# Kernel optimization log

Measured on AMD Instinct MI355X. Metric: run time of the kernel, lower is better.

Reference implementation:

```python
import jax, jax.numpy as jnp
import numpy as np

B, S, D_EMBED, D_HIDDEN = 4, 256, 300, 300
C = 5.0  # frozen tanh-scaling constant


def setup_inputs() -> dict:
    key = jax.random.key(0)
    ks = jax.random.split(key, 8)
    w = 0.05  # ~xavier scale for 300x300
    return {
        "inputs": jax.random.normal(ks[0], (B, S, D_EMBED), jnp.float32),
        "rep_mask": jax.random.randint(ks[1], (B, S), 0, 2, jnp.int32),
        "W_fc": jax.random.normal(ks[2], (D_HIDDEN, D_EMBED), jnp.float32) * w,
        "b_fc": jnp.zeros((D_HIDDEN,), jnp.float32),
        "W1": jax.random.normal(ks[3], (D_HIDDEN, D_HIDDEN), jnp.float32) * w,
        "W2": jax.random.normal(ks[4], (D_HIDDEN, D_HIDDEN), jnp.float32) * w,
        "b1": jnp.zeros((D_HIDDEN,), jnp.float32),
        "W_f1": jax.random.normal(ks[5], (D_HIDDEN, D_HIDDEN), jnp.float32) * w,
        "W_f2": jax.random.normal(ks[6], (D_HIDDEN, D_HIDDEN), jnp.float32) * w,
        "b_f": jnp.zeros((D_HIDDEN,), jnp.float32),
    }


def _disa_fwd(inputs, rep_mask_f, W_fc, b_fc, W1, W2, b1, W_f1, W_f2, b_f):
    n_seq = inputs.shape[1]
    # forward direction mask: attend to strictly later positions (triu, diag=1)
    direct = jnp.triu(jnp.ones((n_seq, n_seq), inputs.dtype), k=1)
    # mask[b,i,j] = rep_mask[b,j] * direct[i,j], shape [B,S,S,1]
    mask = (rep_mask_f[:, None, :] * direct[None]) [..., None]

    rep_map = jax.nn.elu(jnp.einsum('bse,he->bsh', inputs, W_fc) + b_fc)  # [B,S,D]
    dep = jnp.einsum('bsh,gh->bsg', rep_map, W1)   # dependent (token j)
    head = jnp.einsum('bsh,gh->bsg', rep_map, W2)  # head (token i)

    # logits[b,i,j,d]
    logits = C * jnp.tanh((dep[:, None, :, :] + head[:, :, None, :] + b1) / C)

    # hand-rolled masked softmax over dim=2 (j), faithful to original
    masked = logits * mask
    mx = jnp.max(masked, axis=2, keepdims=True)
    exps = jnp.exp(masked - mx) * mask
    sums = jnp.sum(exps, axis=2, keepdims=True)
    sums = sums + (sums == 0).astype(logits.dtype)
    attn = (exps / (sums + 1e-20)) * mask

    attn_result = jnp.sum(attn * rep_map[:, None, :, :], axis=2)  # [B,S,D]

    gate = jax.nn.sigmoid(
        jnp.einsum('bsh,gh->bsg', rep_map, W_f1)
        + jnp.einsum('bsh,gh->bsg', attn_result, W_f2)
        + b_f
    )
    out = gate * rep_map + (1.0 - gate) * attn_result
    return out * rep_mask_f[..., None]


def reference(inputs, rep_mask, W_fc, b_fc, W1, W2, b1, W_f1, W_f2, b_f):
    rep_mask_f = rep_mask.astype(inputs.dtype)
    return _disa_fwd(inputs, rep_mask_f, W_fc, b_fc, W1, W2, b1, W_f1, W_f2, b_f)
```

## Files before the change

### kernel.cpp

```cpp
#include <hip/hip_runtime.h>
#include <hip/hip_bf16.h>

#define Dx 300
#define Mx 1024

#define OFF_REP    0
#define OFF_DEP    307200
#define OFF_HEAD   614400
#define OFF_ATTN   921600
#define U_BASE     1228800
#define REPB       0
#define ATB        327680
#define WPACK      655360
#define WP1        655360
#define WP2        757760
#define WPF1       860160
#define WPF2       962560

typedef __attribute__((ext_vector_type(8))) short short8;
typedef __attribute__((ext_vector_type(4))) float f32x4;

union S8 { unsigned int u[4]; unsigned short s[8]; short8 v; };

__device__ __forceinline__ float bf2f(unsigned short u) {
    union { unsigned int i; float f; } v; v.i = ((unsigned int)u) << 16; return v.f;
}
__device__ __forceinline__ unsigned short f2bf(float x) {
    union { float f; unsigned int i; } u; u.f = x;
    return (unsigned short)((u.i + 0x8000u) >> 16);
}
__device__ __forceinline__ int detect_bf16(const void* w) {
    const unsigned short* u = (const unsigned short*)w;
    int ok = 1;
    #pragma unroll
    for (int t = 0; t < 64; ++t) { float v = bf2f(u[t]); ok &= (fabsf(v) < 1.0f) ? 1 : 0; }
    return ok;
}
__device__ __forceinline__ float ldf(const void* p, int idx, int isbf) {
    return isbf ? bf2f(((const unsigned short*)p)[idx]) : ((const float*)p)[idx];
}

__device__ __forceinline__ void load8f(const float* rowp, int kb, int kmax,
                                       int valid, float* x) {
    if (valid && kb + 8 <= kmax) {
        float4 a = *(const float4*)(rowp + kb);
        float4 b = *(const float4*)(rowp + kb + 4);
        x[0]=a.x; x[1]=a.y; x[2]=a.z; x[3]=a.w;
        x[4]=b.x; x[5]=b.y; x[6]=b.z; x[7]=b.w;
    } else {
        #pragma unroll
        for (int j = 0; j < 8; ++j) {
            int k = kb + j;
            x[j] = (valid && k < kmax) ? rowp[k] : 0.f;
        }
    }
}
__device__ __forceinline__ short8 pack8(const float* x) {
    S8 H;
    #pragma unroll
    for (int p = 0; p < 4; ++p) {
        union { float f; unsigned int i; } a, b;
        a.f = x[2*p]; b.f = x[2*p+1];
        H.u[p] = ((a.i + 0x8000u) >> 16) | ((b.i + 0x8000u) & 0xFFFF0000u);
    }
    return H.v;
}
__device__ __forceinline__ short8 load8bf(const unsigned short* rowp, int kb,
                                          int kmax, int valid) {
    S8 R;
    if (valid && kb + 8 <= kmax) {
        ushort4 a = *(const ushort4*)(rowp + kb);
        ushort4 b = *(const ushort4*)(rowp + kb + 4);
        R.s[0]=a.x; R.s[1]=a.y; R.s[2]=a.z; R.s[3]=a.w;
        R.s[4]=b.x; R.s[5]=b.y; R.s[6]=b.z; R.s[7]=b.w;
    } else {
        #pragma unroll
        for (int j = 0; j < 8; ++j) {
            int k = kb + j;
            R.s[j] = (valid && k < kmax) ? rowp[k] : (unsigned short)0;
        }
    }
    return R.v;
}
__device__ __forceinline__ short8 loadB(const void* W, int row, int kb, int isbf,
                                        int valid) {
    if (isbf) return load8bf((const unsigned short*)W + row * 300, kb, 300, valid);
    float t[8];
    load8f((const float*)W + row * 300, kb, 300, valid, t);
    return pack8(t);
}

__global__ __launch_bounds__(256) void k_mm1(
        const void* __restrict__ Xv, const void* __restrict__ Wfc,
        const void* __restrict__ bfc, const void* __restrict__ W1,
        const void* __restrict__ W2,  const void* __restrict__ Wf1,
        const void* __restrict__ Wf2, float* __restrict__ ws) {
    __shared__ int s_isbf;
    if (threadIdx.x == 0) s_isbf = detect_bf16(Wfc);
    __syncthreads();
    const int isbf = s_isbf;
    const int tid = threadIdx.x;
    unsigned short* U = (unsigned short*)(ws + U_BASE);

    if (blockIdx.x >= 320) {
        const unsigned int idx = (blockIdx.x - 320) * 256 + tid;
        const unsigned int mi = idx / 102400;
        const unsigned int rem = idx - mi * 102400;
        const int row = rem / 320, k = rem - (rem / 320) * 320;
        const void* src = (mi == 0) ? W1 : (mi == 1) ? W2 : (mi == 2) ? Wf1 : Wf2;
        float v = (row < 300 && k < 300) ? ldf(src, row * 300 + k, isbf) : 0.f;
        U[WPACK + idx] = f2bf(v);
        return;
    }

    const int w = tid >> 6, l = tid & 63;
    const int mt = blockIdx.x / 5, nt = blockIdx.x % 5;
    const int m0 = mt * 16, lm = l & 15, koff = (l >> 4) * 8;
    const int nrow = nt * 64 + w * 16 + lm;
    const int bval = nrow < 300;
    const int ncl = bval ? nrow : 0;
    f32x4 acc = {0.f, 0.f, 0.f, 0.f};
    if (isbf) {
        const unsigned short* Xp = (const unsigned short*)Xv + (m0 + lm) * 300;
        #pragma unroll
        for (int ks = 0; ks < 10; ++ks) {
            short8 a = load8bf(Xp, ks*32 + koff, 300, 1);
            short8 b = loadB(Wfc, ncl, ks*32 + koff, 1, bval);
            acc = __builtin_amdgcn_mfma_f32_16x16x32_bf16(a, b, acc, 0, 0, 0);
        }
    } else {
        const float* Xp = (const float*)Xv + (m0 + lm) * 300;
        #pragma unroll
        for (int ks = 0; ks < 10; ++ks) {
            float t[8]; load8f(Xp, ks*32 + koff, 300, 1, t);
            short8 a = pack8(t);
            short8 b = loadB(Wfc, ncl, ks*32 + koff, 0, bval);
            acc = __builtin_amdgcn_mfma_f32_16x16x32_bf16(a, b, acc, 0, 0, 0);
        }
    }
    if (bval) {
        float bb = ldf(bfc, nrow, isbf);
        #pragma unroll
        for (int r = 0; r < 4; ++r) {
            int mg = m0 + (l >> 4) * 4 + r;
            float v = acc[r] + bb;
            v = v > 0.f ? v : (__expf(v) - 1.f);
            ws[OFF_REP + mg * 300 + nrow] = v;
            U[REPB + mg * 320 + nrow] = f2bf(v);
        }
    } else {
        #pragma unroll
        for (int r = 0; r < 4; ++r) {
            int mg = m0 + (l >> 4) * 4 + r;
            U[REPB + mg * 320 + nrow] = 0;
        }
    }
}

__global__ __launch_bounds__(256) void k_mm2(
        const void* __restrict__ b1, const void* __restrict__ Wdet,
        float* __restrict__ ws) {
    __shared__ int s_isbf;
    if (threadIdx.x == 0) s_isbf = detect_bf16(Wdet);
    __syncthreads();
    const int isbf = s_isbf;
    const int tid = threadIdx.x, w = tid >> 6, l = tid & 63;
    const int mt = blockIdx.x / 10, nt = blockIdx.x % 10;
    const int m0 = mt * 16, lm = l & 15, koff = (l >> 4) * 8;
    const int ng = nt * 64 + w * 16 + lm;
    const int wsel = ng < 320;
    const int wrow = wsel ? ng : ng - 320;
    const unsigned short* U = (const unsigned short*)(ws + U_BASE);
    const unsigned short* ap = U + REPB + (m0 + lm) * 320 + koff;
    const unsigned short* bp = U + (wsel ? WP1 : WP2) + wrow * 320 + koff;
    f32x4 acc = {0.f, 0.f, 0.f, 0.f};
    #pragma unroll
    for (int ks = 0; ks < 10; ++ks) {
        short8 a = *(const short8*)(ap + ks * 32);
        short8 b = *(const short8*)(bp + ks * 32);
        acc = __builtin_amdgcn_mfma_f32_16x16x32_bf16(a, b, acc, 0, 0, 0);
    }
    if (ng < 300) {
        float bb = ldf(b1, ng, isbf);
        #pragma unroll
        for (int r = 0; r < 4; ++r) {
            int mg = m0 + (l >> 4) * 4 + r;
            ws[OFF_DEP + mg * 300 + ng] = __expf(0.4f * (acc[r] + bb));
        }
    } else if (ng >= 320 && ng < 620) {
        #pragma unroll
        for (int r = 0; r < 4; ++r) {
            int mg = m0 + (l >> 4) * 4 + r;
            ws[OFF_HEAD + mg * 300 + (ng - 320)] = acc[r];
        }
    }
}

__global__ __launch_bounds__(320) void k_attn(
        float* __restrict__ ws, const int* __restrict__ mask) {
    const float* exd  = ws + OFF_DEP;
    const float* head = ws + OFF_HEAD;
    const float* rep  = ws + OFF_REP;
    unsigned short* U = (unsigned short*)(ws + U_BASE);
    __shared__ unsigned short vlist[256];
    __shared__ int s_cnt, s_st0, s_st1;
    const int blk = blockIdx.x;
    const int b = blk >> 7;
    const int tile = blk & 127;
    const int uu = tile >> 1;
    const int i0 = (tile & 1) ? (254 - 2 * uu) : (2 * uu);
    const int tid = threadIdx.x;

    if (tid < 64) {
        int basec = 0, st0 = 0, st1 = 0;
        #pragma unroll
        for (int c = 0; c < 4; ++c) {
            const int j = c * 64 + tid;
            const int mv = mask[b * 256 + j] != 0;
            unsigned long long bal = __ballot(mv);
            int pos = basec + __popcll(bal & ((1ull << tid) - 1ull));
            if (mv) vlist[pos] = (unsigned short)j;
            if (tid == 0) {
                int lim0 = i0 - c * 64;
                if (lim0 >= 0)
                    st0 += __popcll(bal & (lim0 >= 63 ? ~0ull : ((2ull << lim0) - 1ull)));
                int lim1 = i0 + 1 - c * 64;
                if (lim1 >= 0)
                    st1 += __popcll(bal & (lim1 >= 63 ? ~0ull : ((2ull << lim1) - 1ull)));
            }
            basec += __popcll(bal);
        }
        if (tid == 0) { s_cnt = basec; s_st0 = st0; s_st1 = st1; }
    }
    __syncthreads();
    const int d = tid;
    const int base = b * 256;
    if (d >= 300) {
        U[ATB + (base + i0) * 320 + d] = 0;
        U[ATB + (base + i0 + 1) * 320 + d] = 0;
        return;
    }
    const int cnt = s_cnt, st0 = s_st0, st1 = s_st1;

    const float hv0 = head[(base + i0) * Dx + d];
    const float hv1 = head[(base + i0 + 1) * Dx + d];
    const float pw0 = __expf(0.4f * hv0);
    const float pw1 = __expf(0.4f * hv1);

    const float* ep = exd + base * Dx + d;
    const float* rp = rep + base * Dx + d;
    float s0 = 0.f, r0 = 0.f, s1 = 0.f, r1 = 0.f;
    if (st1 > st0) {
        const int j = vlist[st0];
        float ex = ep[j * Dx];
        float rv = rp[j * Dx];
        float u0 = fmaf(ex, pw0, 1.0f);
        float e0 = __expf(-10.0f * __builtin_amdgcn_rcpf(u0));
        s0 += e0; r0 = fmaf(e0, rv, r0);
    }
    #pragma unroll 4
    for (int t = st1; t < cnt; ++t) {
        const int j = vlist[t];
        float ex = ep[j * Dx];
        float rv = rp[j * Dx];
        float u0 = fmaf(ex, pw0, 1.0f);
        float u1 = fmaf(ex, pw1, 1.0f);
        float e0 = __expf(-10.0f * __builtin_amdgcn_rcpf(u0));
        float e1 = __expf(-10.0f * __builtin_amdgcn_rcpf(u1));
        s0 += e0; r0 = fmaf(e0, rv, r0);
        s1 += e1; r1 = fmaf(e1, rv, r1);
    }
    const float den0 = s0 + (s0 == 0.f ? 1.f : 0.f) + 1e-20f;
    const float den1 = s1 + (s1 == 0.f ? 1.f : 0.f) + 1e-20f;
    const float a0 = r0 / den0, a1 = r1 / den1;
    ws[OFF_ATTN + (base + i0) * Dx + d]     = a0;
    ws[OFF_ATTN + (base + i0 + 1) * Dx + d] = a1;
    U[ATB + (base + i0) * 320 + d]     = f2bf(a0);
    U[ATB + (base + i0 + 1) * 320 + d] = f2bf(a1);
}

__global__ __launch_bounds__(256) void k_mm3(
        const void* __restrict__ bfv, const void* __restrict__ Wdet,
        const int* __restrict__ mask, float* __restrict__ ws,
        void* __restrict__ outv) {
    __shared__ int s_isbf;
    if (threadIdx.x == 0) s_isbf = detect_bf16(Wdet);
    __syncthreads();
    const int isbf = s_isbf;
    const int tid = threadIdx.x, w = tid >> 6, l = tid & 63;
    const int mt = blockIdx.x / 5, nt = blockIdx.x % 5;
    const int m0 = mt * 16, lm = l & 15, koff = (l >> 4) * 8;
    const int nrow = nt * 64 + w * 16 + lm;
    const unsigned short* U = (const unsigned short*)(ws + U_BASE);
    const unsigned short* a1p = U + REPB + (m0 + lm) * 320 + koff;
    const unsigned short* a2p = U + ATB  + (m0 + lm) * 320 + koff;
    const unsigned short* b1p = U + WPF1 + nrow * 320 + koff;
    const unsigned short* b2p = U + WPF2 + nrow * 320 + koff;
    f32x4 acc = {0.f, 0.f, 0.f, 0.f};
    #pragma unroll
    for (int ks = 0; ks < 10; ++ks) {
        short8 a = *(const short8*)(a1p + ks * 32);
        short8 b = *(const short8*)(b1p + ks * 32);
        acc = __builtin_amdgcn_mfma_f32_16x16x32_bf16(a, b, acc, 0, 0, 0);
    }
    #pragma unroll
    for (int ks = 0; ks < 10; ++ks) {
        short8 a = *(const short8*)(a2p + ks * 32);
        short8 b = *(const short8*)(b2p + ks * 32);
        acc = __builtin_amdgcn_mfma_f32_16x16x32_bf16(a, b, acc, 0, 0, 0);
    }
    if (nrow < 300) {
        float bb = ldf(bfv, nrow, isbf);
        #pragma unroll
        for (int r = 0; r < 4; ++r) {
            int mg = m0 + (l >> 4) * 4 + r;
            float gp = acc[r] + bb;
            float gate = 1.0f / (1.0f + __expf(-gp));
            float rv = ws[OFF_REP  + mg * 300 + nrow];
            float av = ws[OFF_ATTN + mg * 300 + nrow];
            float res = (gate * rv + (1.0f - gate) * av) * (float)mask[mg];
            if (isbf) ((__hip_bfloat16*)outv)[mg * 300 + nrow] = __float2bfloat16(res);
            else      ((float*)outv)[mg * 300 + nrow] = res;
        }
    }
}

extern "C" void kernel_launch(void* const* d_in, const int* in_sizes, int n_in,
                              void* d_out, int out_size, void* d_ws, size_t ws_size,
                              hipStream_t stream) {
    const void* X   = d_in[0];
    const int*  msk = (const int*)d_in[1];
    const void* Wfc = d_in[2];
    const void* bfc = d_in[3];
    const void* W1  = d_in[4];
    const void* W2  = d_in[5];
    const void* b1  = d_in[6];
    const void* Wf1 = d_in[7];
    const void* Wf2 = d_in[8];
    const void* bfv = d_in[9];
    float* ws = (float*)d_ws;

    hipLaunchKernelGGL(k_mm1,  dim3(1920), dim3(256), 0, stream,
                       X, Wfc, bfc, W1, W2, Wf1, Wf2, ws);
    hipLaunchKernelGGL(k_mm2,  dim3(640), dim3(256), 0, stream, b1, Wfc, ws);
    hipLaunchKernelGGL(k_attn, dim3(512), dim3(320), 0, stream, ws, msk);
    hipLaunchKernelGGL(k_mm3,  dim3(320), dim3(256), 0, stream,
                       bfv, Wfc, msk, ws, d_out);
}
```

Before: 125.0 us.

## Fuse four kernels into one persistent kernel with software grid barriers

Result: slower. 476.5 us (+281.2%).

```diff
diff --git a/kernel.cpp b/kernel.cpp
--- a/kernel.cpp
+++ b/kernel.cpp
@@ -2,7 +2,6 @@
 #include <hip/hip_bf16.h>
 
 #define Dx 300
-#define Mx 1024
 
 #define OFF_REP    0
 #define OFF_DEP    307200
@@ -16,6 +15,7 @@
 #define WP2        757760
 #define WPF1       860160
 #define WPF2       962560
+#define SYNC_FOFF  2000000
 
 typedef __attribute__((ext_vector_type(8))) short short8;
 typedef __attribute__((ext_vector_type(4))) float f32x4;
@@ -90,237 +90,274 @@
     return pack8(t);
 }
 
-__global__ __launch_bounds__(256) void k_mm1(
-        const void* __restrict__ Xv, const void* __restrict__ Wfc,
-        const void* __restrict__ bfc, const void* __restrict__ W1,
-        const void* __restrict__ W2,  const void* __restrict__ Wf1,
-        const void* __restrict__ Wf2, float* __restrict__ ws) {
+__device__ __forceinline__ void gbar(float* ws, int idx, int nblk) {
+    __syncthreads();
+    if (threadIdx.x == 0) {
+        int* s = (int*)(ws + SYNC_FOFF) + idx * 32;
+        int a = __hip_atomic_fetch_add(s, 1, __ATOMIC_ACQ_REL,
+                                       __HIP_MEMORY_SCOPE_AGENT);
+        if (a == nblk - 1) {
+            __hip_atomic_store(s + 16, 1, __ATOMIC_RELEASE,
+                               __HIP_MEMORY_SCOPE_AGENT);
+        } else {
+            int t = 0;
+            while (__hip_atomic_load(s + 16, __ATOMIC_ACQUIRE,
+                                     __HIP_MEMORY_SCOPE_AGENT) == 0) {
+                __builtin_amdgcn_s_sleep(2);
+                if (++t > 400000) break;
+            }
+        }
+    }
+    __syncthreads();
+}
+
+__global__ __launch_bounds__(320, 4) void k_fused(
+        const void* __restrict__ Xv, const int* __restrict__ mask,
+        const void* __restrict__ Wfc, const void* __restrict__ bfc,
+        const void* __restrict__ W1,  const void* __restrict__ W2,
+        const void* __restrict__ b1v, const void* __restrict__ Wf1,
+        const void* __restrict__ Wf2, const void* __restrict__ bfv,
+        float* __restrict__ ws, void* __restrict__ outv) {
     __shared__ int s_isbf;
-    if (threadIdx.x == 0) s_isbf = detect_bf16(Wfc);
+    __shared__ unsigned short vlist[256];
+    __shared__ int s_cnt, s_st0, s_st1;
+
+    const int tid = threadIdx.x;
+    const int blk = blockIdx.x;
+    if (tid == 0) s_isbf = detect_bf16(Wfc);
     __syncthreads();
     const int isbf = s_isbf;
-    const int tid = threadIdx.x;
     unsigned short* U = (unsigned short*)(ws + U_BASE);
 
-    if (blockIdx.x >= 320) {
-        const unsigned int idx = (blockIdx.x - 320) * 256 + tid;
-        const unsigned int mi = idx / 102400;
-        const unsigned int rem = idx - mi * 102400;
-        const int row = rem / 320, k = rem - (rem / 320) * 320;
-        const void* src = (mi == 0) ? W1 : (mi == 1) ? W2 : (mi == 2) ? Wf1 : Wf2;
-        float v = (row < 300 && k < 300) ? ldf(src, row * 300 + k, isbf) : 0.f;
-        U[WPACK + idx] = f2bf(v);
-        return;
-    }
-
-    const int w = tid >> 6, l = tid & 63;
-    const int mt = blockIdx.x / 5, nt = blockIdx.x % 5;
-    const int m0 = mt * 16, lm = l & 15, koff = (l >> 4) * 8;
-    const int nrow = nt * 64 + w * 16 + lm;
-    const int bval = nrow < 300;
-    const int ncl = bval ? nrow : 0;
-    f32x4 acc = {0.f, 0.f, 0.f, 0.f};
-    if (isbf) {
-        const unsigned short* Xp = (const unsigned short*)Xv + (m0 + lm) * 300;
+    if (blk < 320) {
+        if (tid < 256) {
+            const int w = tid >> 6, l = tid & 63;
+            const int mt = blk / 5, nt = blk % 5;
+            const int m0 = mt * 16, lm = l & 15, koff = (l >> 4) * 8;
+            const int nrow = nt * 64 + w * 16 + lm;
+            const int bval = nrow < 300;
+            const int ncl = bval ? nrow : 0;
+            f32x4 acc = {0.f, 0.f, 0.f, 0.f};
+            if (isbf) {
+                const unsigned short* Xp = (const unsigned short*)Xv + (m0 + lm) * 300;
+                #pragma unroll
+                for (int ks = 0; ks < 10; ++ks) {
+                    short8 a = load8bf(Xp, ks*32 + koff, 300, 1);
+                    short8 b = loadB(Wfc, ncl, ks*32 + koff, 1, bval);
+                    acc = __builtin_amdgcn_mfma_f32_16x16x32_bf16(a, b, acc, 0, 0, 0);
+                }
+            } else {
+                const float* Xp = (const float*)Xv + (m0 + lm) * 300;
+                #pragma unroll
+                for (int ks = 0; ks < 10; ++ks) {
+                    float t[8]; load8f(Xp, ks*32 + koff, 300, 1, t);
+                    short8 a = pack8(t);
+                    short8 b = loadB(Wfc, ncl, ks*32 + koff, 0, bval);
+                    acc = __builtin_amdgcn_mfma_f32_16x16x32_bf16(a, b, acc, 0, 0, 0);
+                }
+            }
+            if (bval) {
+                float bb = ldf(bfc, nrow, isbf);
+                #pragma unroll
+                for (int r = 0; r < 4; ++r) {
+                    int mg = m0 + (l >> 4) * 4 + r;
+                    float v = acc[r] + bb;
+                    v = v > 0.f ? v : (__expf(v) - 1.f);
+                    ws[OFF_REP + mg * 300 + nrow] = v;
+                    U[REPB + mg * 320 + nrow] = f2bf(v);
+                }
+            } else {
+                #pragma unroll
+                for (int r = 0; r < 4; ++r) {
+                    int mg = m0 + (l >> 4) * 4 + r;
+                    U[REPB + mg * 320 + nrow] = 0;
+                }
+            }
+        }
+    } else {
+        const int pid = (blk - 320) * 320 + tid;
+        const int row = pid / 320, k = pid - row * 320;
+        const int inb = (row < 300) & (k < 300);
+        const int off = row * 300 + k;
+        const void* srcs[4] = {W1, W2, Wf1, Wf2};
+        #pragma unroll
+        for (int c = 0; c < 4; ++c) {
+            float v = inb ? ldf(srcs[c], off, isbf) : 0.f;
+            U[WPACK + c * 102400 + pid] = f2bf(v);
+        }
+    }
+    gbar(ws, 0, 640);
+
+    if (tid < 256) {
+        const int w = tid >> 6, l = tid & 63;
+        const int mt = blk / 10, nt = blk % 10;
+        const int m0 = mt * 16, lm = l & 15, koff = (l >> 4) * 8;
+        const int ng = nt * 64 + w * 16 + lm;
+        const int wsel = ng < 320;
+        const int wrow = wsel ? ng : ng - 320;
+        const unsigned short* Uc = U;
+        const unsigned short* ap = Uc + REPB + (m0 + lm) * 320 + koff;
+        const unsigned short* bp = Uc + (wsel ? WP1 : WP2) + wrow * 320 + koff;
+        f32x4 acc = {0.f, 0.f, 0.f, 0.f};
         #pragma unroll
         for (int ks = 0; ks < 10; ++ks) {
-            short8 a = load8bf(Xp, ks*32 + koff, 300, 1);
-            short8 b = loadB(Wfc, ncl, ks*32 + koff, 1, bval);
+            short8 a = *(const short8*)(ap + ks * 32);
+            short8 b = *(const short8*)(bp + ks * 32);
             acc = __builtin_amdgcn_mfma_f32_16x16x32_bf16(a, b, acc, 0, 0, 0);
         }
-    } else {
-        const float* Xp = (const float*)Xv + (m0 + lm) * 300;
+        if (ng < 300) {
+            float bb = ldf(b1v, ng, isbf);
+            #pragma unroll
+            for (int r = 0; r < 4; ++r) {
+                int mg = m0 + (l >> 4) * 4 + r;
+                ws[OFF_DEP + mg * 300 + ng] = __expf(0.4f * (acc[r] + bb));
+            }
+        } else if (ng >= 320 && ng < 620) {
+            #pragma unroll
+            for (int r = 0; r < 4; ++r) {
+                int mg = m0 + (l >> 4) * 4 + r;
+                ws[OFF_HEAD + mg * 300 + (ng - 320)] = acc[r];
+            }
+        }
+    }
+    gbar(ws, 1, 640);
+
+    if (blk < 512) {
+        const int b = blk >> 7;
+        const int tile = blk & 127;
+        const int uu = tile >> 1;
+        const int i0 = (tile & 1) ? (254 - 2 * uu) : (2 * uu);
+        const int base = b * 256;
+        const int mv0 = mask[base + i0] != 0;
+        const int mv1 = mask[base + i0 + 1] != 0;
+        if ((mv0 | mv1) && tid < 64) {
+            int basec = 0, st0 = 0, st1 = 0;
+            #pragma unroll
+            for (int c = 0; c < 4; ++c) {
+                const int j = c * 64 + tid;
+                const int mv = mask[base + j] != 0;
+                unsigned long long bal = __ballot(mv);
+                int pos = basec + __popcll(bal & ((1ull << tid) - 1ull));
+                if (mv) vlist[pos] = (unsigned short)j;
+                if (tid == 0) {
+                    int lim0 = i0 - c * 64;
+                    if (lim0 >= 0)
+                        st0 += __popcll(bal & (lim0 >= 63 ? ~0ull : ((2ull << lim0) - 1ull)));
+                    int lim1 = i0 + 1 - c * 64;
+                    if (lim1 >= 0)
+                        st1 += __popcll(bal & (lim1 >= 63 ? ~0ull : ((2ull << lim1) - 1ull)));
+                }
+                basec += __popcll(bal);
+            }
+            if (tid == 0) { s_cnt = basec; s_st0 = st0; s_st1 = st1; }
+        }
+        __syncthreads();
+        const int d = tid;
+        if (d >= 300) {
+            U[ATB + (base + i0) * 320 + d] = 0;
+            U[ATB + (base + i0 + 1) * 320 + d] = 0;
+        } else if (mv0 & mv1) {
+            const int cnt = s_cnt, st0 = s_st0, st1 = s_st1;
+            const float* headp = ws + OFF_HEAD;
+            const float hv0 = headp[(base + i0) * Dx + d];
+            const float hv1 = headp[(base + i0 + 1) * Dx + d];
+            const float pw0 = __expf(0.4f * hv0);
+            const float pw1 = __expf(0.4f * hv1);
+            const float* ep = ws + OFF_DEP + base * Dx + d;
+            const float* rp = ws + OFF_REP + base * Dx + d;
+            float s0 = 0.f, r0 = 0.f, s1 = 0.f, r1 = 0.f;
+            if (st1 > st0) {
+                const int j = vlist[st0];
+                float ex = ep[j * Dx];
+                float rv = rp[j * Dx];
+                float u0 = fmaf(ex, pw0, 1.0f);
+                float e0 = __expf(-10.0f * __builtin_amdgcn_rcpf(u0));
+                s0 += e0; r0 = fmaf(e0, rv, r0);
+            }
+            #pragma unroll 4
+            for (int t = st1; t < cnt; ++t) {
+                const int j = vlist[t];
+                float ex = ep[j * Dx];
+                float rv = rp[j * Dx];
+                float u0 = fmaf(ex, pw0, 1.0f);
+                float u1 = fmaf(ex, pw1, 1.0f);
+                float e0 = __expf(-10.0f * __builtin_amdgcn_rcpf(u0));
+                float e1 = __expf(-10.0f * __builtin_amdgcn_rcpf(u1));
+                s0 += e0; r0 = fmaf(e0, rv, r0);
+                s1 += e1; r1 = fmaf(e1, rv, r1);
+            }
+            const float den0 = s0 + (s0 == 0.f ? 1.f : 0.f) + 1e-20f;
+            const float den1 = s1 + (s1 == 0.f ? 1.f : 0.f) + 1e-20f;
+            const float a0 = r0 / den0, a1 = r1 / den1;
+            ws[OFF_ATTN + (base + i0) * Dx + d]     = a0;
+            ws[OFF_ATTN + (base + i0 + 1) * Dx + d] = a1;
+            U[ATB + (base + i0) * 320 + d]     = f2bf(a0);
+            U[ATB + (base + i0 + 1) * 320 + d] = f2bf(a1);
+        } else if (mv0 | mv1) {
+            const int cnt = s_cnt;
+            const int ia  = mv0 ? i0 : (i0 + 1);
+            const int sta = mv0 ? s_st0 : s_st1;
+            const float hv = (ws + OFF_HEAD)[(base + ia) * Dx + d];
+            const float pw = __expf(0.4f * hv);
+            const float* ep = ws + OFF_DEP + base * Dx + d;
+            const float* rp = ws + OFF_REP + base * Dx + d;
+            float s = 0.f, r = 0.f;
+            #pragma unroll 4
+            for (int t = sta; t < cnt; ++t) {
+                const int j = vlist[t];
+                float ex = ep[j * Dx];
+                float rv = rp[j * Dx];
+                float u0 = fmaf(ex, pw, 1.0f);
+                float e  = __expf(-10.0f * __builtin_amdgcn_rcpf(u0));
+                s += e; r = fmaf(e, rv, r);
+            }
+            const float den = s + (s == 0.f ? 1.f : 0.f) + 1e-20f;
+            const float a = r / den;
+            ws[OFF_ATTN + (base + ia) * Dx + d] = a;
+            U[ATB + (base + ia) * 320 + d] = f2bf(a);
+        }
+    }
+    gbar(ws, 2, 640);
+
+    if (blk < 320 && tid < 256) {
+        const int w = tid >> 6, l = tid & 63;
+        const int mt = blk / 5, nt = blk % 5;
+        const int m0 = mt * 16, lm = l & 15, koff = (l >> 4) * 8;
+        const int nrow = nt * 64 + w * 16 + lm;
+        const unsigned short* Uc = U;
+        const unsigned short* a1p = Uc + REPB + (m0 + lm) * 320 + koff;
+        const unsigned short* a2p = Uc + ATB  + (m0 + lm) * 320 + koff;
+        const unsigned short* b1p = Uc + WPF1 + nrow * 320 + koff;
+        const unsigned short* b2p = Uc + WPF2 + nrow * 320 + koff;
+        f32x4 acc = {0.f, 0.f, 0.f, 0.f};
         #pragma unroll
         for (int ks = 0; ks < 10; ++ks) {
-            float t[8]; load8f(Xp, ks*32 + koff, 300, 1, t);
-            short8 a = pack8(t);
-            short8 b = loadB(Wfc, ncl, ks*32 + koff, 0, bval);
+            short8 a = *(const short8*)(a1p + ks * 32);
+            short8 b = *(const short8*)(b1p + ks * 32);
             acc = __builtin_amdgcn_mfma_f32_16x16x32_bf16(a, b, acc, 0, 0, 0);
         }
-    }
-    if (bval) {
-        float bb = ldf(bfc, nrow, isbf);
-        #pragma unroll
-        for (int r = 0; r < 4; ++r) {
-            int mg = m0 + (l >> 4) * 4 + r;
-            float v = acc[r] + bb;
-            v = v > 0.f ? v : (__expf(v) - 1.f);
-            ws[OFF_REP + mg * 300 + nrow] = v;
-            U[REPB + mg * 320 + nrow] = f2bf(v);
-        }
-    } else {
-        #pragma unroll
-        for (int r = 0; r < 4; ++r) {
-            int mg = m0 + (l >> 4) * 4 + r;
-            U[REPB + mg * 320 + nrow] = 0;
-        }
-    }
-}
-
-__global__ __launch_bounds__(256) void k_mm2(
-        const void* __restrict__ b1, const void* __restrict__ Wdet,
-        float* __restrict__ ws) {
-    __shared__ int s_isbf;
-    if (threadIdx.x == 0) s_isbf = detect_bf16(Wdet);
-    __syncthreads();
-    const int isbf = s_isbf;
-    const int tid = threadIdx.x, w = tid >> 6, l = tid & 63;
-    const int mt = blockIdx.x / 10, nt = blockIdx.x % 10;
-    const int m0 = mt * 16, lm = l & 15, koff = (l >> 4) * 8;
-    const int ng = nt * 64 + w * 16 + lm;
-    const int wsel = ng < 320;
-    const int wrow = wsel ? ng : ng - 320;
-    const unsigned short* U = (const unsigned short*)(ws + U_BASE);
-    const unsigned short* ap = U + REPB + (m0 + lm) * 320 + koff;
-    const unsigned short* bp = U + (wsel ? WP1 : WP2) + wrow * 320 + koff;
-    f32x4 acc = {0.f, 0.f, 0.f, 0.f};
-    #pragma unroll
-    for (int ks = 0; ks < 10; ++ks) {
-        short8 a = *(const short8*)(ap + ks * 32);
-        short8 b = *(const short8*)(bp + ks * 32);
-        acc = __builtin_amdgcn_mfma_f32_16x16x32_bf16(a, b, acc, 0, 0, 0);
-    }
-    if (ng < 300) {
-        float bb = ldf(b1, ng, isbf);
-        #pragma unroll
-        for (int r = 0; r < 4; ++r) {
-            int mg = m0 + (l >> 4) * 4 + r;
-            ws[OFF_DEP + mg * 300 + ng] = __expf(0.4f * (acc[r] + bb));
-        }
-    } else if (ng >= 320 && ng < 620) {
-        #pragma unroll
-        for (int r = 0; r < 4; ++r) {
-            int mg = m0 + (l >> 4) * 4 + r;
-            ws[OFF_HEAD + mg * 300 + (ng - 320)] = acc[r];
-        }
-    }
-}
-
-__global__ __launch_bounds__(320) void k_attn(
-        float* __restrict__ ws, const int* __restrict__ mask) {
-    const float* exd  = ws + OFF_DEP;
-    const float* head = ws + OFF_HEAD;
-    const float* rep  = ws + OFF_REP;
-    unsigned short* U = (unsigned short*)(ws + U_BASE);
-    __shared__ unsigned short vlist[256];
-    __shared__ int s_cnt, s_st0, s_st1;
-    const int blk = blockIdx.x;
-    const int b = blk >> 7;
-    const int tile = blk & 127;
-    const int uu = tile >> 1;
-    const int i0 = (tile & 1) ? (254 - 2 * uu) : (2 * uu);
-    const int tid = threadIdx.x;
-
-    if (tid < 64) {
-        int basec = 0, st0 = 0, st1 = 0;
-        #pragma unroll
-        for (int c = 0; c < 4; ++c) {
-            const int j = c * 64 + tid;
-            const int mv = mask[b * 256 + j] != 0;
-            unsigned long long bal = __ballot(mv);
-            int pos = basec + __popcll(bal & ((1ull << tid) - 1ull));
-            if (mv) vlist[pos] = (unsigned short)j;
-            if (tid == 0) {
-                int lim0 = i0 - c * 64;
-                if (lim0 >= 0)
-                    st0 += __popcll(bal & (lim0 >= 63 ? ~0ull : ((2ull << lim0) - 1ull)));
-                int lim1 = i0 + 1 - c * 64;
-                if (lim1 >= 0)
-                    st1 += __popcll(bal & (lim1 >= 63 ? ~0ull : ((2ull << lim1) - 1ull)));
-            }
-            basec += __popcll(bal);
-        }
-        if (tid == 0) { s_cnt = basec; s_st0 = st0; s_st1 = st1; }
-    }
-    __syncthreads();
-    const int d = tid;
-    const int base = b * 256;
-    if (d >= 300) {
-        U[ATB + (base + i0) * 320 + d] = 0;
-        U[ATB + (base + i0 + 1) * 320 + d] = 0;
-        return;
-    }
-    const int cnt = s_cnt, st0 = s_st0, st1 = s_st1;
-
-    const float hv0 = head[(base + i0) * Dx + d];
-    const float hv1 = head[(base + i0 + 1) * Dx + d];
-    const float pw0 = __expf(0.4f * hv0);
-    const float pw1 = __expf(0.4f * hv1);
-
-    const float* ep = exd + base * Dx + d;
-    const float* rp = rep + base * Dx + d;
-    float s0 = 0.f, r0 = 0.f, s1 = 0.f, r1 = 0.f;
-    if (st1 > st0) {
-        const int j = vlist[st0];
-        float ex = ep[j * Dx];
-        float rv = rp[j * Dx];
-        float u0 = fmaf(ex, pw0, 1.0f);
-        float e0 = __expf(-10.0f * __builtin_amdgcn_rcpf(u0));
-        s0 += e0; r0 = fmaf(e0, rv, r0);
-    }
-    #pragma unroll 4
-    for (int t = st1; t < cnt; ++t) {
-        const int j = vlist[t];
-        float ex = ep[j * Dx];
-        float rv = rp[j * Dx];
-        float u0 = fmaf(ex, pw0, 1.0f);
-        float u1 = fmaf(ex, pw1, 1.0f);
-        float e0 = __expf(-10.0f * __builtin_amdgcn_rcpf(u0));
-        float e1 = __expf(-10.0f * __builtin_amdgcn_rcpf(u1));
-        s0 += e0; r0 = fmaf(e0, rv, r0);
-        s1 += e1; r1 = fmaf(e1, rv, r1);
-    }
-    const float den0 = s0 + (s0 == 0.f ? 1.f : 0.f) + 1e-20f;
-    const float den1 = s1 + (s1 == 0.f ? 1.f : 0.f) + 1e-20f;
-    const float a0 = r0 / den0, a1 = r1 / den1;
-    ws[OFF_ATTN + (base + i0) * Dx + d]     = a0;
-    ws[OFF_ATTN + (base + i0 + 1) * Dx + d] = a1;
-    U[ATB + (base + i0) * 320 + d]     = f2bf(a0);
-    U[ATB + (base + i0 + 1) * 320 + d] = f2bf(a1);
-}
-
-__global__ __launch_bounds__(256) void k_mm3(
-        const void* __restrict__ bfv, const void* __restrict__ Wdet,
-        const int* __restrict__ mask, float* __restrict__ ws,
-        void* __restrict__ outv) {
-    __shared__ int s_isbf;
-    if (threadIdx.x == 0) s_isbf = detect_bf16(Wdet);
-    __syncthreads();
-    const int isbf = s_isbf;
-    const int tid = threadIdx.x, w = tid >> 6, l = tid & 63;
-    const int mt = blockIdx.x / 5, nt = blockIdx.x % 5;
-    const int m0 = mt * 16, lm = l & 15, koff = (l >> 4) * 8;
-    const int nrow = nt * 64 + w * 16 + lm;
-    const unsigned short* U = (const unsigned short*)(ws + U_BASE);
-    const unsigned short* a1p = U + REPB + (m0 + lm) * 320 + koff;
-    const unsigned short* a2p = U + ATB  + (m0 + lm) * 320 + koff;
-    const unsigned short* b1p = U + WPF1 + nrow * 320 + koff;
-    const unsigned short* b2p = U + WPF2 + nrow * 320 + koff;
-    f32x4 acc = {0.f, 0.f, 0.f, 0.f};
-    #pragma unroll
-    for (int ks = 0; ks < 10; ++ks) {
-        short8 a = *(const short8*)(a1p + ks * 32);
-        short8 b = *(const short8*)(b1p + ks * 32);
-        acc = __builtin_amdgcn_mfma_f32_16x16x32_bf16(a, b, acc, 0, 0, 0);
-    }
-    #pragma unroll
-    for (int ks = 0; ks < 10; ++ks) {
-        short8 a = *(const short8*)(a2p + ks * 32);
-        short8 b = *(const short8*)(b2p + ks * 32);
-        acc = __builtin_amdgcn_mfma_f32_16x16x32_bf16(a, b, acc, 0, 0, 0);
-    }
-    if (nrow < 300) {
-        float bb = ldf(bfv, nrow, isbf);
-        #pragma unroll
-        for (int r = 0; r < 4; ++r) {
-            int mg = m0 + (l >> 4) * 4 + r;
-            float gp = acc[r] + bb;
-            float gate = 1.0f / (1.0f + __expf(-gp));
-            float rv = ws[OFF_REP  + mg * 300 + nrow];
-            float av = ws[OFF_ATTN + mg * 300 + nrow];
-            float res = (gate * rv + (1.0f - gate) * av) * (float)mask[mg];
-            if (isbf) ((__hip_bfloat16*)outv)[mg * 300 + nrow] = __float2bfloat16(res);
-            else      ((float*)outv)[mg * 300 + nrow] = res;
+        #pragma unroll
+        for (int ks = 0; ks < 10; ++ks) {
+            short8 a = *(const short8*)(a2p + ks * 32);
+            short8 b = *(const short8*)(b2p + ks * 32);
+            acc = __builtin_amdgcn_mfma_f32_16x16x32_bf16(a, b, acc, 0, 0, 0);
+        }
+        if (nrow < 300) {
+            float bb = ldf(bfv, nrow, isbf);
+            #pragma unroll
+            for (int r = 0; r < 4; ++r) {
+                int mg = m0 + (l >> 4) * 4 + r;
+                float res = 0.f;
+                if (mask[mg]) {
+                    float gp = acc[r] + bb;
+                    float gate = 1.0f / (1.0f + __expf(-gp));
+                    float rv = ws[OFF_REP  + mg * 300 + nrow];
+                    float av = ws[OFF_ATTN + mg * 300 + nrow];
+                    res = gate * rv + (1.0f - gate) * av;
+                }
+                if (isbf) ((__hip_bfloat16*)outv)[mg * 300 + nrow] = __float2bfloat16(res);
+                else      ((float*)outv)[mg * 300 + nrow] = res;
+            }
         }
     }
 }
@@ -340,10 +377,8 @@
     const void* bfv = d_in[9];
     float* ws = (float*)d_ws;
 
-    hipLaunchKernelGGL(k_mm1,  dim3(1920), dim3(256), 0, stream,
-                       X, Wfc, bfc, W1, W2, Wf1, Wf2, ws);
-    hipLaunchKernelGGL(k_mm2,  dim3(640), dim3(256), 0, stream, b1, Wfc, ws);
-    hipLaunchKernelGGL(k_attn, dim3(512), dim3(320), 0, stream, ws, msk);
-    hipLaunchKernelGGL(k_mm3,  dim3(320), dim3(256), 0, stream,
-                       bfv, Wfc, msk, ws, d_out);
-}
+    hipMemsetAsync((char*)d_ws + (size_t)SYNC_FOFF * sizeof(float), 0, 512, stream);
+
+    hipLaunchKernelGGL(k_fused, dim3(640), dim3(320), 0, stream,
+                       X, msk, Wfc, bfc, W1, W2, b1, Wf1, Wf2, bfv, ws, d_out);
+}
```
